# Kernel optimization log

Measured on AMD Instinct MI355X. Metric: run time of the kernel, lower is better.

Reference implementation:

```python
import jax, jax.numpy as jnp
import numpy as np

B, S, DIM = 2, 2048, 4096
H, KV, HD = 32, 8, 128
REP = H // KV
SCALE = HD ** -0.5
ROPE_THETA = 10000.0


def setup_inputs() -> dict:
    key = jax.random.key(0)
    ks = jax.random.split(key, 6)
    x = jax.random.normal(ks[0], (B, S, DIM), dtype=jnp.float32)
    # weights stored [in, out]; y = x @ W matches nn.Linear(in,out,bias=False)
    wq = jax.random.normal(ks[1], (DIM, H * HD), dtype=jnp.float32) * (DIM ** -0.5)
    wk = jax.random.normal(ks[2], (DIM, KV * HD), dtype=jnp.float32) * (DIM ** -0.5)
    wv = jax.random.normal(ks[3], (DIM, KV * HD), dtype=jnp.float32) * (DIM ** -0.5)
    wo = jax.random.normal(ks[4], (H * HD, DIM), dtype=jnp.float32) * ((H * HD) ** -0.5)
    # RoPE tables: angle[t, j] = t * theta^(-2j/hd)
    inv_freq = 1.0 / (ROPE_THETA ** (np.arange(0, HD, 2, dtype=np.float32) / HD))
    t = np.arange(S, dtype=np.float32)
    angles = np.outer(t, inv_freq)  # [S, HD/2]
    freqs_cos = jnp.asarray(np.cos(angles), dtype=jnp.float32)
    freqs_sin = jnp.asarray(np.sin(angles), dtype=jnp.float32)
    # causal additive mask
    neg = jnp.finfo(jnp.float32).min
    mask = jnp.where(jnp.tril(jnp.ones((S, S), dtype=bool)), 0.0, neg).astype(jnp.float32)
    positions = jnp.arange(S, dtype=jnp.int64)
    return {"x": x, "wq": wq, "wk": wk, "wv": wv, "wo": wo,
            "freqs_cos": freqs_cos, "freqs_sin": freqs_sin,
            "mask": mask, "positions": positions}


def _rope(t, cos, sin):
    # t: [b, s, h, hd]; cos/sin: [s, hd/2]
    b, s, h, hd = t.shape
    tr = t.reshape(b, s, h, hd // 2, 2)
    tre, tim = tr[..., 0], tr[..., 1]
    c = cos[None, :, None, :]
    sn = sin[None, :, None, :]
    out_re = tre * c - tim * sn
    out_im = tre * sn + tim * c
    return jnp.stack([out_re, out_im], axis=-1).reshape(b, s, h, hd)


def reference(x, wq, wk, wv, wo, freqs_cos, freqs_sin, mask, positions):
    b, s, _ = x.shape
    xq = (x @ wq).reshape(b, s, H, HD)
    xk = (x @ wk).reshape(b, s, KV, HD)
    xv = (x @ wv).reshape(b, s, KV, HD)
    xq = _rope(xq, freqs_cos, freqs_sin)
    xk = _rope(xk, freqs_cos, freqs_sin)
    # GQA without materializing repeated KV: group query heads by kv head
    q = xq.transpose(0, 2, 1, 3).reshape(b, KV, REP, s, HD)  # [b,g,r,s,d]
    k = xk.transpose(0, 2, 1, 3)                              # [b,g,s,d]
    v = xv.transpose(0, 2, 1, 3)                              # [b,g,s,d]
    scores = jnp.einsum('bgrqd,bgkd->bgrqk', q, k) * SCALE
    scores = scores + mask[None, None, None, :, :]
    probs = jax.nn.softmax(scores.astype(jnp.float32), axis=-1).astype(q.dtype)
    out = jnp.einsum('bgrqk,bgkd->bgrqd', probs, v)           # [b,g,r,s,d]
    out = out.reshape(b, H, s, HD).transpose(0, 2, 1, 3).reshape(b, s, H * HD)
    return out @ wo
```

## Files before the change

kernel.cpp:

```cpp
#include <hip/hip_runtime.h>
#include <math.h>

#define B_ 2
#define S_ 2048
#define DIM_ 4096
#define H_ 32
#define KV_ 8
#define HD_ 128
#define SCALE_ 0.08838834764831844f
#define QSCALE_ 0.12751744154254998f
#define KVOFF_ 4194304

typedef unsigned short u16;
typedef __attribute__((ext_vector_type(8))) short bf16x8;
typedef __attribute__((ext_vector_type(4))) float f32x4;
typedef __attribute__((ext_vector_type(16))) float f32x16;
typedef __attribute__((ext_vector_type(8))) unsigned short u16x8;
typedef __attribute__((ext_vector_type(4))) unsigned short u16x4;

__device__ __forceinline__ u16 f2b(float f) {
  union { float f; unsigned u; } v; v.f = f;
  unsigned r = v.u + 0x7fffu + ((v.u >> 16) & 1u);
  return (u16)(r >> 16);
}
__device__ __forceinline__ float b2f(u16 h) {
  union { unsigned u; float f; } v; v.u = ((unsigned)h) << 16;
  return v.f;
}
__device__ __forceinline__ unsigned cvt_pk_bf16(float lo, float hi) {
  unsigned r;
  asm("v_cvt_pk_bf16_f32 %0, %1, %2" : "=v"(r) : "v"(lo), "v"(hi));
  return r;
}
__device__ __forceinline__ void async_copy16(const void* g, void* l) {
  __builtin_amdgcn_global_load_lds(
      (const __attribute__((address_space(1))) void*)g,
      (__attribute__((address_space(3))) void*)l, 16, 0, 0);
}
__device__ __forceinline__ void bar() {
  asm volatile("s_barrier" ::: "memory");
}

__global__ __launch_bounds__(256) void cvt_bf16(const float* __restrict__ in,
                                                u16* __restrict__ out, int n4) {
  int i = blockIdx.x * 256 + threadIdx.x;
  if (i >= n4) return;
  float4 v = ((const float4*)in)[i];
  u16x4 o; o[0] = f2b(v.x); o[1] = f2b(v.y); o[2] = f2b(v.z); o[3] = f2b(v.w);
  ((u16x4*)out)[i] = o;
}

__global__ __launch_bounds__(256) void transpose_cvt(
    const float* __restrict__ W, u16* __restrict__ WT, int K, int N) {
  __shared__ float Ts[64][65];
  const int tid = threadIdx.x;
  const int n0 = blockIdx.x * 64, k0 = blockIdx.y * 64;
#pragma unroll
  for (int p = 0; p < 4; ++p) {
    int r = p * 16 + (tid >> 4), c = (tid & 15) * 4;
    float4 v = *(const float4*)(W + (size_t)(k0 + r) * N + n0 + c);
    Ts[r][c] = v.x; Ts[r][c + 1] = v.y; Ts[r][c + 2] = v.z; Ts[r][c + 3] = v.w;
  }
  __syncthreads();
#pragma unroll
  for (int p = 0; p < 4; ++p) {
    int n = p * 16 + (tid >> 4), kq = (tid & 15) * 4;
    u16x4 o;
    o[0] = f2b(Ts[kq + 0][n]); o[1] = f2b(Ts[kq + 1][n]);
    o[2] = f2b(Ts[kq + 2][n]); o[3] = f2b(Ts[kq + 3][n]);
    *(u16x4*)(WT + (size_t)(n0 + n) * K + k0 + kq) = o;
  }
}

__global__ __launch_bounds__(256) void transpose_v(const u16* __restrict__ V,
                                                   u16* __restrict__ Vt) {
  __shared__ u16 Ts[64][72];
  const int tid = threadIdx.x;
  const int s0 = blockIdx.x * 64, d0 = blockIdx.y * 64, hb = blockIdx.z;
  const u16* src = V + ((size_t)hb * S_ + s0) * HD_ + d0;
#pragma unroll
  for (int p = 0; p < 2; ++p) {
    int r = p * 32 + (tid >> 3), seg = (tid & 7) * 8;
    u16x8 v = *(const u16x8*)(src + (size_t)r * HD_ + seg);
#pragma unroll
    for (int j = 0; j < 8; ++j) Ts[r][seg + j] = v[j];
  }
  __syncthreads();
  u16* dst = Vt + ((size_t)hb * HD_ + d0) * S_ + s0;
#pragma unroll
  for (int p = 0; p < 2; ++p) {
    int d = p * 32 + (tid >> 3), seg = (tid & 7) * 8;
    u16x8 o;
#pragma unroll
    for (int j = 0; j < 8; ++j) o[j] = Ts[seg + j][d];
    *(u16x8*)(dst + (size_t)d * S_ + seg) = o;
  }
}

__global__ __launch_bounds__(256) void rope_bf16(unsigned* __restrict__ T,
                                                 const float* __restrict__ cs,
                                                 const float* __restrict__ sn,
                                                 int total, float scale) {
  int idx = blockIdx.x * 256 + threadIdx.x;
  if (idx >= total) return;
  int i = idx & 63, s = (idx >> 6) & (S_ - 1);
  float c = cs[s * 64 + i], si = sn[s * 64 + i];
  unsigned v = T[idx];
  float re = b2f((u16)(v & 0xffffu)), im = b2f((u16)(v >> 16));
  float ore = (re * c - im * si) * scale, oim = (re * si + im * c) * scale;
  T[idx] = (unsigned)f2b(ore) | ((unsigned)f2b(oim) << 16);
}

template <int OUT_MODE>
__global__ __launch_bounds__(256) void gemm_bf16(
    const u16* __restrict__ A, const u16* __restrict__ Bt,
    void* __restrict__ Cout, int M, int N, int K, int heads) {
  __shared__ u16 As[128 * 64];
  __shared__ u16 Bs[128 * 64];
  const int tid = threadIdx.x, lane = tid & 63;
  const int wbase = tid & ~63;
  const int o = blockIdx.y * gridDim.x + blockIdx.x;
  const int q8 = (gridDim.x * gridDim.y) >> 3;
  const int p = (o & 7) * q8 + (o >> 3);
  const int row0 = (p / gridDim.x) * 128, col0 = (p % gridDim.x) * 128;
  const int wm = ((tid >> 6) >> 1) * 64, wn = ((tid >> 6) & 1) * 64;

  f32x4 acc[4][4];
#pragma unroll
  for (int i = 0; i < 4; ++i)
#pragma unroll
    for (int j = 0; j < 4; ++j) acc[i][j] = (f32x4){0.f, 0.f, 0.f, 0.f};

  const int nk = K >> 6;
  for (int kt = 0; kt < nk; ++kt) {
    const int k0 = kt << 6;
#pragma unroll
    for (int i = 0; i < 4; ++i) {
      int g = i * 256 + tid;
      int r = g >> 3, ss = (g & 7) ^ (r & 7);
      async_copy16(A + (size_t)(row0 + r) * K + k0 + ss * 8,
                   (char*)As + (i * 256 + wbase) * 16);
    }
#pragma unroll
    for (int i = 0; i < 4; ++i) {
      int g = i * 256 + tid;
      int r = g >> 3, ss = (g & 7) ^ (r & 7);
      async_copy16(Bt + (size_t)(col0 + r) * K + k0 + ss * 8,
                   (char*)Bs + (i * 256 + wbase) * 16);
    }
    __syncthreads();
#pragma unroll
    for (int ks = 0; ks < 2; ++ks) {
      bf16x8 af[4], bf[4];
#pragma unroll
      for (int mi = 0; mi < 4; ++mi) {
        int r = wm + mi * 16 + (lane & 15);
        int off = (ks * 64 + ((lane >> 4) << 4)) ^ ((r & 7) << 4);
        af[mi] = *(const bf16x8*)((const char*)As + r * 128 + off);
      }
#pragma unroll
      for (int ni = 0; ni < 4; ++ni) {
        int r = wn + ni * 16 + (lane & 15);
        int off = (ks * 64 + ((lane >> 4) << 4)) ^ ((r & 7) << 4);
        bf[ni] = *(const bf16x8*)((const char*)Bs + r * 128 + off);
      }
#pragma unroll
      for (int mi = 0; mi < 4; ++mi)
#pragma unroll
        for (int ni = 0; ni < 4; ++ni)
          acc[mi][ni] = __builtin_amdgcn_mfma_f32_16x16x32_bf16(
              af[mi], bf[ni], acc[mi][ni], 0, 0, 0);
    }
    __syncthreads();
  }

#pragma unroll
  for (int mi = 0; mi < 4; ++mi)
#pragma unroll
    for (int ni = 0; ni < 4; ++ni) {
      int mb = row0 + wm + mi * 16 + ((lane >> 4) << 2);
      int n = col0 + wn + ni * 16 + (lane & 15);
#pragma unroll
      for (int r = 0; r < 4; ++r) {
        int m = mb + r;
        float v = acc[mi][ni][r];
        if (OUT_MODE == 0) {
          ((float*)Cout)[(size_t)m * N + n] = v;
        } else if (OUT_MODE == 1) {
          int b = m >> 11, s = m & (S_ - 1);
          int h = n >> 7, d = n & (HD_ - 1);
          ((u16*)Cout)[(((size_t)(b * heads + h)) * S_ + s) * HD_ + d] = f2b(v);
        } else {
          int b = m >> 11, s = m & (S_ - 1);
          int hh = n >> 7, d = n & (HD_ - 1);
          size_t base = (size_t)(hh >> 3) * KVOFF_;
          ((u16*)Cout)[base + (((size_t)(b * 8 + (hh & 7))) * S_ + s) * HD_ + d] =
              f2b(v);
        }
      }
    }
}

template <int OUT_MODE>
__global__ __launch_bounds__(512) void gemm256(
    const u16* __restrict__ A, const u16* __restrict__ Bt,
    void* __restrict__ Cout, int M, int N, int K, int heads) {
  __shared__ u16 lds[65536];
  char* const ldsb = (char*)lds;
  const int tid = threadIdx.x, lane = tid & 63, wid = tid >> 6;
  const int q = lane & 15, g = lane >> 4;
  const int wm = wid >> 2, wn = wid & 3;
  const int o = blockIdx.y * gridDim.x + blockIdx.x;
  const int q8 = (gridDim.x * gridDim.y) >> 3;
  const int p = (o & 7) * q8 + (o >> 3);
  const int row0 = (p / gridDim.x) * 256, col0 = (p % gridDim.x) * 256;
  const int nk = K >> 6, nh = nk << 2;

  const u16* srcA[2];
  const u16* srcB[2];
#pragma unroll
  for (int u = 0; u < 2; ++u) {
    int j = u * 512 + tid;
    int row = ((j >> 3) << 1) + ((j >> 2) & 1);
    int colg = (j & 3) ^ ((j >> 3) & 3);
    srcA[u] = A + (size_t)(row0 + row) * K + colg * 8;
    srcB[u] = Bt + (size_t)(col0 + row) * K + colg * 8;
  }

  auto STAGE = [&](int h) {
    if (h >= nh) return;
    int tau = h >> 2, ks = (h >> 1) & 1, op = h & 1;
    int slot = (2 * tau + ks) & 3;
    int koff = tau * 64 + ks * 32;
    char* lbase = ldsb + op * 65536 + slot * 16384 + wid * 1024;
#pragma unroll
    for (int u = 0; u < 2; ++u)
      async_copy16((op ? srcB[u] : srcA[u]) + koff, lbase + u * 8192);
  };

  int aread[8], bread[4];
#pragma unroll
  for (int mi = 0; mi < 8; ++mi) {
    int row = wm * 128 + mi * 16 + q;
    aread[mi] = (row >> 1) * 128 + (row & 1) * 64 + ((g ^ ((row >> 1) & 3)) << 4);
  }
#pragma unroll
  for (int ni = 0; ni < 4; ++ni) {
    int row = wn * 64 + ni * 16 + q;
    bread[ni] = (row >> 1) * 128 + (row & 1) * 64 + ((g ^ ((row >> 1) & 3)) << 4);
  }

  f32x4 acc[8][4];
#pragma unroll
  for (int i = 0; i < 8; ++i)
#pragma unroll
    for (int j = 0; j < 4; ++j) acc[i][j] = (f32x4){0.f, 0.f, 0.f, 0.f};

  auto RDA = [&](bf16x8* d, const char* s, int ob) {
#pragma unroll
    for (int i = 0; i < 4; ++i) d[i] = *(const bf16x8*)(s + aread[ob + i]);
  };
  auto RDB = [&](bf16x8* d, const char* s) {
#pragma unroll
    for (int i = 0; i < 4; ++i) d[i] = *(const bf16x8*)(s + bread[i]);
  };
  auto MFMA16 = [&](int mo, bf16x8* af, bf16x8* bfr) {
    __builtin_amdgcn_s_setprio(1);
#pragma unroll
    for (int mi = 0; mi < 4; ++mi)
#pragma unroll
      for (int ni = 0; ni < 4; ++ni)
        acc[mo + mi][ni] = __builtin_amdgcn_mfma_f32_16x16x32_bf16(
            af[mi], bfr[ni], acc[mo + mi][ni], 0, 0, 0);
    __builtin_amdgcn_s_setprio(0);
  };

#pragma unroll
  for (int h = 0; h < 6; ++h) STAGE(h);
  asm volatile("s_waitcnt vmcnt(4)" ::: "memory");
  bar();
  bf16x8 afc[4], afn[4], bfc[4], bfn[4];
  RDA(afc, ldsb, 0);
  RDB(bfc, ldsb + 65536);

  for (int t = 0; t < nk; ++t) {
    const int s0 = (2 * t) & 3, s1 = (2 * t + 1) & 3;
    const char* As0 = ldsb + s0 * 16384;
    const char* Bs1 = ldsb + 65536 + s1 * 16384;
    const char* As1 = ldsb + s1 * 16384;

    STAGE(4 * t + 6);
    bar();
    MFMA16(0, afc, bfc);
    RDA(afn, As0, 4);
    bar();

    STAGE(4 * t + 7);
    bar();
    MFMA16(4, afn, bfc);
    RDA(afc, As1, 0);
    RDB(bfn, Bs1);
    bar();

    STAGE(4 * t + 8);
    bar();
    MFMA16(0, afc, bfn);
    RDA(afn, As1, 4);
    bar();

    STAGE(4 * t + 9);
    bar();
    MFMA16(4, afn, bfn);
    if (t < nk - 2)
      asm volatile("s_waitcnt vmcnt(4)" ::: "memory");
    else if (t == nk - 2)
      asm volatile("s_waitcnt vmcnt(0)" ::: "memory");
    if (t < nk - 1) {
      const char* As0n = ldsb + ((2 * t + 2) & 3) * 16384;
      const char* Bs0n = ldsb + 65536 + ((2 * t + 2) & 3) * 16384;
      RDA(afc, As0n, 0);
      RDB(bfc, Bs0n);
    }
    bar();
  }

#pragma unroll
  for (int mi = 0; mi < 8; ++mi)
#pragma unroll
    for (int ni = 0; ni < 4; ++ni) {
      int mb = row0 + wm * 128 + mi * 16 + (g << 2);
      int n = col0 + wn * 64 + ni * 16 + q;
#pragma unroll
      for (int r = 0; r < 4; ++r) {
        int m = mb + r;
        float v = acc[mi][ni][r];
        if (OUT_MODE == 0) {
          ((float*)Cout)[(size_t)m * N + n] = v;
        } else {
          int b = m >> 11, s = m & (S_ - 1);
          int h = n >> 7, d = n & (HD_ - 1);
          ((u16*)Cout)[(((size_t)(b * heads + h)) * S_ + s) * HD_ + d] = f2b(v);
        }
      }
    }
}

__global__ __launch_bounds__(256, 2) void attn_mfma(
    const u16* __restrict__ Qb, const u16* __restrict__ Kb,
    const u16* __restrict__ Vt, u16* __restrict__ AO,
    const float* __restrict__ fc, const float* __restrict__ fs) {
  __shared__ u16 Ks[2][64 * 128];
  __shared__ u16 Vs[2][128 * 64];

  const int tid = threadIdx.x, lane = tid & 63, wid = tid >> 6;
  const int wbase = tid & ~63;
  const int o = blockIdx.x + (blockIdx.y << 3) + (blockIdx.z << 8);
  const int pid = o >> 6, h = o & 31, b = (o >> 5) & 1;
  const int kvh = h >> 2;
  const int l31 = lane & 31, hi = lane >> 5;

  const u16* Kbase = Kb + ((size_t)(b * KV_ + kvh) * S_) * HD_;
  const u16* Vbase = Vt + ((size_t)(b * KV_ + kvh) * HD_) * S_;

  const u16* Kl[4];
  const u16* Vl[4];
#pragma unroll
  for (int i = 0; i < 4; ++i) {
    int gg = i * 256 + tid;
    int rK = gg >> 4, ssK = (gg & 15) ^ (rK & 7);
    Kl[i] = Kbase + (size_t)rK * HD_ + ssK * 8;
    int rV = gg >> 3, ssV = (gg & 7) ^ (rV & 7);
    Vl[i] = Vbase + (size_t)rV * S_ + ssV * 8;
  }

  auto STAGE_KV = [&](int kt, int buf) {
    const int kv0 = kt * 64;
#pragma unroll
    for (int i = 0; i < 4; ++i)
      async_copy16(Kl[i] + (size_t)kv0 * HD_,
                   (char*)Ks[buf] + (i * 256 + wbase) * 16);
#pragma unroll
    for (int i = 0; i < 4; ++i)
      async_copy16(Vl[i] + kv0, (char*)Vs[buf] + (i * 256 + wbase) * 16);
  };

  for (int half = 0; half < 2; ++half) {
    const int qt = half ? (15 - pid) : pid;
    const int q0 = qt * 128;
    const int qg = q0 + wid * 32 + l31;

    STAGE_KV(0, 0);

    bf16x8 qf[8];
    {
      const u16* qrow = Qb + ((size_t)(b * H_ + h) * S_ + qg) * HD_ + hi * 8;
      const float* cb = fc + qg * 64 + hi * 4;
      const float* sb = fs + qg * 64 + hi * 4;
#pragma unroll
      for (int ks = 0; ks < 8; ++ks) {
        u16x8 v = *(const u16x8*)(qrow + ks * 16);
        float4 cv = *(const float4*)(cb + ks * 8);
        float4 sv = *(const float4*)(sb + ks * 8);
        unsigned w[4];
#pragma unroll
        for (int j = 0; j < 4; ++j) {
          float c = ((const float*)&cv)[j] * QSCALE_;
          float s = ((const float*)&sv)[j] * QSCALE_;
          float re = b2f((u16)v[2 * j]), im = b2f((u16)v[2 * j + 1]);
          w[j] = cvt_pk_bf16(re * c - im * s, re * s + im * c);
        }
        union { unsigned u[4]; bf16x8 q; } cvt;
        cvt.u[0] = w[0]; cvt.u[1] = w[1]; cvt.u[2] = w[2]; cvt.u[3] = w[3];
        qf[ks] = cvt.q;
      }
    }

    f32x16 oacc[4];
#pragma unroll
    for (int i = 0; i < 4; ++i)
#pragma unroll
      for (int j = 0; j < 16; ++j) oacc[i][j] = 0.f;
    float mrow = -3e38f, lrow = 0.f;

    __syncthreads();

    const int nkt = 2 * qt + 2;
    for (int kt = 0; kt < nkt; ++kt) {
      const int cur = kt & 1;
      if (kt + 1 < nkt) STAGE_KV(kt + 1, cur ^ 1);
      const char* Kc = (const char*)Ks[cur];
      const char* Vc = (const char*)Vs[cur];
      const int kv0 = kt * 64;

      f32x16 sacc[2];
#pragma unroll
      for (int kf = 0; kf < 2; ++kf)
#pragma unroll
        for (int j = 0; j < 16; ++j) sacc[kf][j] = 0.f;
#pragma unroll
      for (int ks = 0; ks < 8; ++ks) {
#pragma unroll
        for (int kf = 0; kf < 2; ++kf) {
          const int arow = kf * 32 + l31;
          bf16x8 kfrag = *(const bf16x8*)(
              Kc + arow * 256 + ((((ks * 2 + hi) << 4)) ^ ((arow & 7) << 4)));
          sacc[kf] = __builtin_amdgcn_mfma_f32_32x32x16_bf16(kfrag, qf[ks],
                                                             sacc[kf], 0, 0, 0);
        }
      }

      if (kv0 + 63 > q0 + wid * 32) {
#pragma unroll
        for (int kf = 0; kf < 2; ++kf)
#pragma unroll
          for (int r = 0; r < 16; ++r) {
            int kg = kv0 + kf * 32 + (r & 3) + 8 * (r >> 2) + 4 * hi;
            if (kg > qg) sacc[kf][r] = -3e38f;
          }
      }

      float rmax = -3e38f;
#pragma unroll
      for (int kf = 0; kf < 2; ++kf)
#pragma unroll
        for (int r = 0; r < 16; ++r) rmax = fmaxf(rmax, sacc[kf][r]);
      rmax = fmaxf(rmax, __shfl_xor(rmax, 32, 64));
      const bool defer = __all(rmax - mrow <= 11.5f);
      float mnew, fsc;
      if (defer) {
        mnew = mrow; fsc = 1.0f;
      } else {
        mnew = fmaxf(mrow, rmax); fsc = exp2f(mrow - mnew);
      }
      mrow = mnew;
      float psum = 0.f;
#pragma unroll
      for (int kf = 0; kf < 2; ++kf)
#pragma unroll
        for (int r = 0; r < 16; ++r) {
          float p = exp2f(sacc[kf][r] - mnew);
          sacc[kf][r] = p;
          psum += p;
        }
      psum += __shfl_xor(psum, 32, 64);
      lrow = lrow * fsc + psum;

      if (!defer) {
#pragma unroll
        for (int r = 0; r < 16; ++r) {
          float fr = __shfl(fsc, (r & 3) + 8 * (r >> 2) + 4 * hi, 64);
#pragma unroll
          for (int df = 0; df < 4; ++df) oacc[df][r] *= fr;
        }
      }

      bf16x8 pa[4];
#pragma unroll
      for (int kf = 0; kf < 2; ++kf) {
        unsigned w0 = cvt_pk_bf16(sacc[kf][0], sacc[kf][1]);
        unsigned w1 = cvt_pk_bf16(sacc[kf][2], sacc[kf][3]);
        unsigned w2 = cvt_pk_bf16(sacc[kf][4], sacc[kf][5]);
        unsigned w3 = cvt_pk_bf16(sacc[kf][6], sacc[kf][7]);
        unsigned w4 = cvt_pk_bf16(sacc[kf][8], sacc[kf][9]);
        unsigned w5 = cvt_pk_bf16(sacc[kf][10], sacc[kf][11]);
        unsigned w6 = cvt_pk_bf16(sacc[kf][12], sacc[kf][13]);
        unsigned w7 = cvt_pk_bf16(sacc[kf][14], sacc[kf][15]);
        asm volatile("v_permlane32_swap_b32 %0, %1" : "+v"(w0), "+v"(w2));
        asm volatile("v_permlane32_swap_b32 %0, %1" : "+v"(w1), "+v"(w3));
        asm volatile("v_permlane32_swap_b32 %0, %1" : "+v"(w4), "+v"(w6));
        asm volatile("v_permlane32_swap_b32 %0, %1" : "+v"(w5), "+v"(w7));
        union { unsigned u[4]; bf16x8 q; } f0, f1;
        f0.u[0] = w0; f0.u[1] = w1; f0.u[2] = w2; f0.u[3] = w3;
        f1.u[0] = w4; f1.u[1] = w5; f1.u[2] = w6; f1.u[3] = w7;
        pa[kf * 2] = f0.q;
        pa[kf * 2 + 1] = f1.q;
      }

#pragma unroll
      for (int ks = 0; ks < 4; ++ks) {
#pragma unroll
        for (int df = 0; df < 4; ++df) {
          const int vrow = df * 32 + l31;
          bf16x8 vf = *(const bf16x8*)(
              Vc + vrow * 128 + ((((ks * 2 + hi) << 4)) ^ ((vrow & 7) << 4)));
          oacc[df] = __builtin_amdgcn_mfma_f32_32x32x16_bf16(pa[ks], vf,
                                                             oacc[df], 0, 0, 0);
        }
      }
      __syncthreads();
    }

    const float linv = 1.f / lrow;
#pragma unroll
    for (int r = 0; r < 16; ++r) {
      const int qloc = (r & 3) + 8 * (r >> 2) + 4 * hi;
      const float invq = __shfl(linv, qloc, 64);
      const int sq = q0 + wid * 32 + qloc;
      u16* dst = AO + (size_t)(b * S_ + sq) * (H_ * HD_) + h * HD_ + l31;
#pragma unroll
      for (int df = 0; df < 4; ++df) dst[df * 32] = f2b(oacc[df][r] * invq);
    }
  }
}

extern "C" void kernel_launch(void* const* d_in, const int* in_sizes, int n_in,
                              void* d_out, int out_size, void* d_ws, size_t ws_size,
                              hipStream_t stream) {
  const float* x  = (const float*)d_in[0];
  const float* wq = (const float*)d_in[1];
  const float* wk = (const float*)d_in[2];
  const float* wv = (const float*)d_in[3];
  const float* wo = (const float*)d_in[4];
  const float* fc = (const float*)d_in[5];
  const float* fs = (const float*)d_in[6];
  float* out = (float*)d_out;

  u16* ws  = (u16*)d_ws;
  u16* wqT = ws;
  u16* VtB = ws;
  u16* xb  = ws + 16777216;
  u16* AOb = xb;
  u16* woT = ws + 33554432;
  u16* Qh  = ws + 50331648;
  u16* wkT = ws + 67108864;
  u16* wvT = ws + 71303168;
  u16* Kh  = ws + 75497472;
  u16* Vh  = ws + 79691776;

  dim3 blk(256);

  cvt_bf16<<<dim3(16384), blk, 0, stream>>>(x, xb, 4194304);
  transpose_cvt<<<dim3(64, 64), blk, 0, stream>>>(wq, wqT, DIM_, H_ * HD_);
  transpose_cvt<<<dim3(16, 64), blk, 0, stream>>>(wk, wkT, DIM_, KV_ * HD_);
  transpose_cvt<<<dim3(16, 64), blk, 0, stream>>>(wv, wvT, DIM_, KV_ * HD_);
  transpose_cvt<<<dim3(64, 64), blk, 0, stream>>>(wo, woT, H_ * HD_, DIM_);

  gemm256<1><<<dim3(16, 16), dim3(512), 0, stream>>>(xb, wqT, Qh, 4096, 4096, 4096, H_);
  gemm_bf16<2><<<dim3(16, 32), blk, 0, stream>>>(xb, wkT, Kh, 4096, 2048, 4096, KV_);

  rope_bf16<<<dim3(8192), blk, 0, stream>>>((unsigned*)Kh, fc, fs, 2097152, 1.0f);

  transpose_v<<<dim3(32, 2, 16), blk, 0, stream>>>(Vh, VtB);

  attn_mfma<<<dim3(8, 32, 2), blk, 0, stream>>>(Qh, Kh, VtB, AOb, fc, fs);

  gemm256<0><<<dim3(16, 16), dim3(512), 0, stream>>>(AOb, woT, out, 4096, 4096, 4096, 0);
}
```

Before: 517.6 us.

## Fuse V transpose into KV GEMM epilogue and tune attention scheduling

The KV projection GEMM now writes V directly in transposed [b,kv,d,s] layout with packed 4-element stores, so the separate transpose_v kernel and the intermediate V buffer are gone. The attention kernel raises wave priority around its MFMA blocks and splits the row-max and row-sum reductions into four independent accumulators to shorten dependency chains. This removes one launch and a full read/write pass over V. The transposed stores stride by S per d, so they are less coalesced than the old row-major writes.

```diff
diff --git a/kernel.cpp b/kernel.cpp
--- a/kernel.cpp
+++ b/kernel.cpp
@@ -9,7 +9,6 @@
 #define HD_ 128
 #define SCALE_ 0.08838834764831844f
 #define QSCALE_ 0.12751744154254998f
-#define KVOFF_ 4194304
 
 typedef unsigned short u16;
 typedef __attribute__((ext_vector_type(8))) short bf16x8;
@@ -69,31 +68,6 @@
     o[0] = f2b(Ts[kq + 0][n]); o[1] = f2b(Ts[kq + 1][n]);
     o[2] = f2b(Ts[kq + 2][n]); o[3] = f2b(Ts[kq + 3][n]);
     *(u16x4*)(WT + (size_t)(n0 + n) * K + k0 + kq) = o;
-  }
-}
-
-__global__ __launch_bounds__(256) void transpose_v(const u16* __restrict__ V,
-                                                   u16* __restrict__ Vt) {
-  __shared__ u16 Ts[64][72];
-  const int tid = threadIdx.x;
-  const int s0 = blockIdx.x * 64, d0 = blockIdx.y * 64, hb = blockIdx.z;
-  const u16* src = V + ((size_t)hb * S_ + s0) * HD_ + d0;
-#pragma unroll
-  for (int p = 0; p < 2; ++p) {
-    int r = p * 32 + (tid >> 3), seg = (tid & 7) * 8;
-    u16x8 v = *(const u16x8*)(src + (size_t)r * HD_ + seg);
-#pragma unroll
-    for (int j = 0; j < 8; ++j) Ts[r][seg + j] = v[j];
-  }
-  __syncthreads();
-  u16* dst = Vt + ((size_t)hb * HD_ + d0) * S_ + s0;
-#pragma unroll
-  for (int p = 0; p < 2; ++p) {
-    int d = p * 32 + (tid >> 3), seg = (tid & 7) * 8;
-    u16x8 o;
-#pragma unroll
-    for (int j = 0; j < 8; ++j) o[j] = Ts[seg + j][d];
-    *(u16x8*)(dst + (size_t)d * S_ + seg) = o;
   }
 }
 
@@ -111,10 +85,9 @@
   T[idx] = (unsigned)f2b(ore) | ((unsigned)f2b(oim) << 16);
 }
 
-template <int OUT_MODE>
-__global__ __launch_bounds__(256) void gemm_bf16(
+__global__ __launch_bounds__(256) void gemm_kv(
     const u16* __restrict__ A, const u16* __restrict__ Bt,
-    void* __restrict__ Cout, int M, int N, int K, int heads) {
+    u16* __restrict__ Kh, u16* __restrict__ Vt, int M, int N, int K) {
   __shared__ u16 As[128 * 64];
   __shared__ u16 Bs[128 * 64];
   const int tid = threadIdx.x, lane = tid & 63;
@@ -178,25 +151,20 @@
   for (int mi = 0; mi < 4; ++mi)
 #pragma unroll
     for (int ni = 0; ni < 4; ++ni) {
-      int mb = row0 + wm + mi * 16 + ((lane >> 4) << 2);
-      int n = col0 + wn + ni * 16 + (lane & 15);
-#pragma unroll
-      for (int r = 0; r < 4; ++r) {
-        int m = mb + r;
-        float v = acc[mi][ni][r];
-        if (OUT_MODE == 0) {
-          ((float*)Cout)[(size_t)m * N + n] = v;
-        } else if (OUT_MODE == 1) {
-          int b = m >> 11, s = m & (S_ - 1);
-          int h = n >> 7, d = n & (HD_ - 1);
-          ((u16*)Cout)[(((size_t)(b * heads + h)) * S_ + s) * HD_ + d] = f2b(v);
-        } else {
-          int b = m >> 11, s = m & (S_ - 1);
-          int hh = n >> 7, d = n & (HD_ - 1);
-          size_t base = (size_t)(hh >> 3) * KVOFF_;
-          ((u16*)Cout)[base + (((size_t)(b * 8 + (hh & 7))) * S_ + s) * HD_ + d] =
-              f2b(v);
-        }
+      const int mb = row0 + wm + mi * 16 + ((lane >> 4) << 2);
+      const int n = col0 + wn + ni * 16 + (lane & 15);
+      const int b = mb >> 11, s0 = mb & (S_ - 1);
+      const int hh = n >> 7, d = n & (HD_ - 1);
+      if (hh < 8) {
+#pragma unroll
+        for (int r = 0; r < 4; ++r)
+          Kh[(((size_t)(b * 8 + hh)) * S_ + s0 + r) * HD_ + d] =
+              f2b(acc[mi][ni][r]);
+      } else {
+        u16x4 ov;
+#pragma unroll
+        for (int r = 0; r < 4; ++r) ov[r] = f2b(acc[mi][ni][r]);
+        *(u16x4*)(Vt + (((size_t)(b * 8 + (hh & 7)) * HD_ + d) * S_ + s0)) = ov;
       }
     }
 }
@@ -437,6 +405,7 @@
       for (int kf = 0; kf < 2; ++kf)
 #pragma unroll
         for (int j = 0; j < 16; ++j) sacc[kf][j] = 0.f;
+      __builtin_amdgcn_s_setprio(1);
 #pragma unroll
       for (int ks = 0; ks < 8; ++ks) {
 #pragma unroll
@@ -448,6 +417,7 @@
                                                              sacc[kf], 0, 0, 0);
         }
       }
+      __builtin_amdgcn_s_setprio(0);
 
       if (kv0 + 63 > q0 + wid * 32) {
 #pragma unroll
@@ -459,11 +429,17 @@
           }
       }
 
-      float rmax = -3e38f;
+      float m0 = -3e38f, m1 = -3e38f, m2 = -3e38f, m3 = -3e38f;
 #pragma unroll
       for (int kf = 0; kf < 2; ++kf)
 #pragma unroll
-        for (int r = 0; r < 16; ++r) rmax = fmaxf(rmax, sacc[kf][r]);
+        for (int r = 0; r < 4; ++r) {
+          m0 = fmaxf(m0, sacc[kf][r]);
+          m1 = fmaxf(m1, sacc[kf][r + 4]);
+          m2 = fmaxf(m2, sacc[kf][r + 8]);
+          m3 = fmaxf(m3, sacc[kf][r + 12]);
+        }
+      float rmax = fmaxf(fmaxf(m0, m1), fmaxf(m2, m3));
       rmax = fmaxf(rmax, __shfl_xor(rmax, 32, 64));
       const bool defer = __all(rmax - mrow <= 11.5f);
       float mnew, fsc;
@@ -473,15 +449,20 @@
         mnew = fmaxf(mrow, rmax); fsc = exp2f(mrow - mnew);
       }
       mrow = mnew;
-      float psum = 0.f;
+      float p0 = 0.f, p1 = 0.f, p2 = 0.f, p3 = 0.f;
 #pragma unroll
       for (int kf = 0; kf < 2; ++kf)
 #pragma unroll
-        for (int r = 0; r < 16; ++r) {
-          float p = exp2f(sacc[kf][r] - mnew);
-          sacc[kf][r] = p;
-          psum += p;
-        }
+        for (int r = 0; r < 4; ++r) {
+          float e0 = exp2f(sacc[kf][r] - mnew);
+          float e1 = exp2f(sacc[kf][r + 4] - mnew);
+          float e2 = exp2f(sacc[kf][r + 8] - mnew);
+          float e3 = exp2f(sacc[kf][r + 12] - mnew);
+          sacc[kf][r] = e0; sacc[kf][r + 4] = e1;
+          sacc[kf][r + 8] = e2; sacc[kf][r + 12] = e3;
+          p0 += e0; p1 += e1; p2 += e2; p3 += e3;
+        }
+      float psum = (p0 + p1) + (p2 + p3);
       psum += __shfl_xor(psum, 32, 64);
       lrow = lrow * fsc + psum;
 
@@ -516,6 +497,7 @@
         pa[kf * 2 + 1] = f1.q;
       }
 
+      __builtin_amdgcn_s_setprio(1);
 #pragma unroll
       for (int ks = 0; ks < 4; ++ks) {
 #pragma unroll
@@ -527,6 +509,7 @@
                                                              oacc[df], 0, 0, 0);
         }
       }
+      __builtin_amdgcn_s_setprio(0);
       __syncthreads();
     }
 
@@ -565,7 +548,6 @@
   u16* wkT = ws + 67108864;
   u16* wvT = ws + 71303168;
   u16* Kh  = ws + 75497472;
-  u16* Vh  = ws + 79691776;
 
   dim3 blk(256);
 
@@ -576,12 +558,10 @@
   transpose_cvt<<<dim3(64, 64), blk, 0, stream>>>(wo, woT, H_ * HD_, DIM_);
 
   gemm256<1><<<dim3(16, 16), dim3(512), 0, stream>>>(xb, wqT, Qh, 4096, 4096, 4096, H_);
-  gemm_bf16<2><<<dim3(16, 32), blk, 0, stream>>>(xb, wkT, Kh, 4096, 2048, 4096, KV_);
+  gemm_kv<<<dim3(16, 32), blk, 0, stream>>>(xb, wkT, Kh, VtB, 4096, 2048, 4096);
 
   rope_bf16<<<dim3(8192), blk, 0, stream>>>((unsigned*)Kh, fc, fs, 2097152, 1.0f);
 
-  transpose_v<<<dim3(32, 2, 16), blk, 0, stream>>>(Vh, VtB);
-
   attn_mfma<<<dim3(8, 32, 2), blk, 0, stream>>>(Qh, Kh, VtB, AOb, fc, fs);
 
   gemm256<0><<<dim3(16, 16), dim3(512), 0, stream>>>(AOb, woT, out, 4096, 4096, 4096, 0);
```

Result: no change. 522.3 us (+0.9%).
